# Kernel optimization log

Measured on AMD Instinct MI355X. Metric: run time of the kernel, lower is better.

## Reference

```python
import jax, jax.numpy as jnp
import numpy as np

MA_K = 25  # moving-average window for temporal pattern decoupling (trend extraction)
BN_EPS = 1e-5


def conv1d(x, w, b, dilation=1, padding=0, groups=1):
    # x: [N, C, L], w: [O, I/groups, K]
    out = jax.lax.conv_general_dilated(
        x, w, window_strides=(1,), padding=[(padding, padding)],
        rhs_dilation=(dilation,), dimension_numbers=("NCH", "OIH", "NCH"),
        feature_group_count=groups)
    if b is not None:
        out = out + b[None, :, None]
    return out


def moving_avg(x):
    # series-decomposition trend: depthwise uniform conv with edge padding
    c = x.shape[1]
    xp = jnp.pad(x, ((0, 0), (0, 0), (MA_K // 2, MA_K // 2)), mode="edge")
    k = jnp.full((c, 1, MA_K), 1.0 / MA_K, dtype=x.dtype)
    return conv1d(xp, k, None, dilation=1, padding=0, groups=c)


def setup_inputs() -> dict:
    key = jax.random.key(0)
    ks = jax.random.split(key, 12)
    B, C, L = 16, 256, 4096
    nb = 4
    c = C // nb  # 64 per branch
    inp = {
        "x": jax.random.normal(ks[0], (B, C, L), dtype=jnp.float32),
        # stacked per-branch Conv1dBlock params (all branches share c)
        "conv_w": jax.random.normal(ks[1], (nb, c, c, 3), dtype=jnp.float32) * 0.05,
        "conv_b": jax.random.normal(ks[2], (nb, c), dtype=jnp.float32) * 0.05,
        "bn_gamma": 1.0 + 0.1 * jax.random.normal(ks[3], (nb, c), dtype=jnp.float32),
        "bn_beta": 0.1 * jax.random.normal(ks[4], (nb, c), dtype=jnp.float32),
        "bn_mean": 0.1 * jax.random.normal(ks[5], (nb, c), dtype=jnp.float32),
        "bn_var": 0.5 + jax.random.uniform(ks[6], (nb, c), dtype=jnp.float32),
        # fusion 1x1 conv: 2C -> C
        "fusion_w": jax.random.normal(ks[7], (C, 2 * C, 1), dtype=jnp.float32) * 0.02,
        "fusion_b": jax.random.normal(ks[8], (C,), dtype=jnp.float32) * 0.02,
        "alpha": jnp.ones((1,), dtype=jnp.float32),
    }
    return inp


def reference(x, conv_w, conv_b, bn_gamma, bn_beta, bn_mean, bn_var,
              fusion_w, fusion_b, alpha):
    nb = conv_w.shape[0]
    parts = jnp.split(x, nb, axis=1)  # equal branch channels (C % nb == 0)
    shorts, longs = [], []
    for i in range(nb):
        d = 2 ** i  # dilation; padding = d keeps length for k=3
        h = conv1d(parts[i], conv_w[i], conv_b[i], dilation=d, padding=d)
        # BatchNorm1d, inference semantics (running stats)
        inv = jax.lax.rsqrt(bn_var[i] + BN_EPS)
        h = (h - bn_mean[i][None, :, None]) * (bn_gamma[i] * inv)[None, :, None] \
            + bn_beta[i][None, :, None]
        h = jax.nn.gelu(h, approximate=False)
        # TemporalPatternDecoupling: long = moving-average trend, short = residual
        l = moving_avg(h)
        s = h - l
        # dim_check AdaptiveAvgPool1d(seq_len) and F.interpolate(size=L) are
        # identity here since every branch already has length L == seq_len
        shorts.append(s)
        longs.append(l)
    # cumulative fuse: short forward, long backward
    for b in range(1, nb):
        shorts[b] = shorts[b] + shorts[b - 1]
    for b in reversed(range(nb - 1)):
        longs[b] = longs[b] + longs[b + 1]
    fused = jnp.concatenate(shorts + longs, axis=1)  # [B, 2C, L]
    out = jax.nn.relu(conv1d(fused, fusion_w, fusion_b))
    return out + alpha[0] * x
```

## Files before the change

kernel.cpp:

```cpp
#include <hip/hip_runtime.h>
#include <math.h>

#define BATCH 16
#define CCH 256
#define LSEQ 4096
#define NB 4
#define CB 64
#define MA_H 12
#define BN_EPS 1e-5f

typedef __attribute__((ext_vector_type(8))) short bf16x8;
typedef __attribute__((ext_vector_type(4))) float f32x4;

__device__ inline float b2f(ushort u) {
    union { uint i; float f; } v; v.i = ((uint)u) << 16; return v.f;
}
__device__ inline ushort f2b(float f) {
    uint x = __float_as_uint(f);
    return (ushort)((x + 0x7FFFu + ((x >> 16) & 1u)) >> 16);
}

__global__ __launch_bounds__(256) void k0w_fusionw(const float* __restrict__ fw,
                                                   ushort* __restrict__ wbf2)
{
    int e = blockIdx.x * 256 + threadIdx.x;
    int o = e >> 6, j = e & 63;
    const float* row = fw + (size_t)o * 512;
    float ws0 = row[j],       ws1 = row[64 + j],
          ws2 = row[128 + j], ws3 = row[192 + j];
    float wl0 = row[256 + j], wl1 = row[320 + j],
          wl2 = row[384 + j], wl3 = row[448 + j];
    float S3 = ws3, S2 = ws2 + S3, S1 = ws1 + S2, S0 = ws0 + S1;
    float L0 = wl0, L1 = L0 + wl1, L2 = L1 + wl2, L3 = L2 + wl3;
    ushort* dst = wbf2 + (size_t)o * 512;
    dst[j]        = f2b(S0); dst[64 + j]  = f2b(S1);
    dst[128 + j]  = f2b(S2); dst[192 + j] = f2b(S3);
    dst[256 + j]  = f2b(L0 - S0); dst[320 + j] = f2b(L1 - S1);
    dst[384 + j]  = f2b(L2 - S2); dst[448 + j] = f2b(L3 - S3);
}

__global__ __launch_bounds__(256) void k0b_convw_branch(
    const float* __restrict__ conv_w, ushort* __restrict__ wbr)
{
    int e = blockIdx.x * 256 + threadIdx.x;
    int i    = e & 63;
    int rest = e >> 6;
    int kk   = rest % 3;
    int orow = rest / 3;
    float v = conv_w[(size_t)orow * 192 + i * 3 + kk];
    wbr[(size_t)orow * 192 + kk * 64 + i] = f2b(v);
}

__global__ __launch_bounds__(256) void k0c_xT(const float* __restrict__ x,
                                              ushort* __restrict__ xT)
{
    const int p0    = blockIdx.x * 64;
    const int batch = blockIdx.y;
    const int tid   = threadIdx.x;

    __shared__ uint ls[256 * 33];

    const float* xb = x + (size_t)batch * CCH * LSEQ;
#pragma unroll
    for (int pass = 0; pass < 16; ++pass) {
        int e  = tid + pass * 256;
        int ch = e >> 4;
        int c4 = e & 15;
        float4 v = *(const float4*)&xb[(size_t)ch * LSEQ + p0 + c4 * 4];
        uint u0 = (uint)f2b(v.x) | ((uint)f2b(v.y) << 16);
        uint u1 = (uint)f2b(v.z) | ((uint)f2b(v.w) << 16);
        ls[ch * 33 + c4 * 2]     = u0;
        ls[ch * 33 + c4 * 2 + 1] = u1;
    }
    __syncthreads();

    const int w = tid >> 6, l = tid & 63;
    const ushort* lsu = (const ushort*)ls;
    ushort* dst = xT + ((size_t)batch * LSEQ + p0) * CCH;
#pragma unroll
    for (int r = 0; r < 16; ++r) {
        int p = w * 16 + r;
#pragma unroll
        for (int q = 0; q < 4; ++q) {
            int ch = l + 64 * q;
            dst[(size_t)p * CCH + ch] = lsu[ch * 66 + p];
        }
    }
}

#define SXA 72
#define SWB 200
__global__ __launch_bounds__(256) void k1_conv_mfma(
    const ushort* __restrict__ xT, const ushort* __restrict__ wbr,
    const float* __restrict__ conv_b, const float* __restrict__ bn_gamma,
    const float* __restrict__ bn_beta, const float* __restrict__ bn_mean,
    const float* __restrict__ bn_var, ushort* __restrict__ hT)
{
    const int tile  = blockIdx.x;
    const int br    = blockIdx.y;
    const int batch = blockIdx.z;
    const int d     = 1 << br;
    const int t0    = tile * 128;
    const int tid   = threadIdx.x;
    const int wm    = tid >> 6;
    const int lane  = tid & 63;
    const int lo    = lane & 15;
    const int hi    = lane >> 4;

    __shared__ ushort xsA[144 * SXA];
    __shared__ ushort wlB[64 * SWB];

    {
        const ushort* xTb = xT + (size_t)batch * LSEQ * CCH + br * CB;
#pragma unroll
        for (int pass = 0; pass < 5; ++pass) {
            int e = tid + pass * 256;
            int p = e >> 3;
            int c = e & 7;
            if (p < 144) {
                int gp = t0 - 8 + p;
                uint4 v = make_uint4(0u, 0u, 0u, 0u);
                if (gp >= 0 && gp < LSEQ)
                    v = *(const uint4*)&xTb[(size_t)gp * CCH + c * 8];
                *(uint4*)&xsA[p * SXA + c * 8] = v;
            }
        }
    }
    {
        const ushort* wrow = wbr + ((size_t)br * CB) * 192;
#pragma unroll
        for (int pass = 0; pass < 6; ++pass) {
            int e = tid + pass * 256;
            int o = e / 24;
            int c = e - o * 24;
            uint4 v = *(const uint4*)&wrow[e * 8];
            *(uint4*)&wlB[o * SWB + c * 8] = v;
        }
    }
    __syncthreads();

    f32x4 acc[2][4];
#pragma unroll
    for (int mi = 0; mi < 2; ++mi)
#pragma unroll
        for (int ni = 0; ni < 4; ++ni) acc[mi][ni] = (f32x4)0.f;

#pragma unroll
    for (int kk = 0; kk < 3; ++kk) {
        const int roff = 8 + (kk - 1) * d;
#pragma unroll
        for (int ks = 0; ks < 2; ++ks) {
            bf16x8 af[2], bfr[4];
#pragma unroll
            for (int mi = 0; mi < 2; ++mi)
                af[mi] = *(const bf16x8*)&xsA[
                    (wm * 32 + mi * 16 + lo + roff) * SXA + ks * 32 + hi * 8];
#pragma unroll
            for (int ni = 0; ni < 4; ++ni)
                bfr[ni] = *(const bf16x8*)&wlB[
                    (ni * 16 + lo) * SWB + kk * 64 + ks * 32 + hi * 8];
#pragma unroll
            for (int mi = 0; mi < 2; ++mi)
#pragma unroll
                for (int ni = 0; ni < 4; ++ni)
                    acc[mi][ni] = __builtin_amdgcn_mfma_f32_16x16x32_bf16(
                        af[mi], bfr[ni], acc[mi][ni], 0, 0, 0);
        }
    }

    __syncthreads();
    ushort* os = xsA;
#pragma unroll
    for (int ni = 0; ni < 4; ++ni) {
        const int o  = ni * 16 + lo;
        const int go = br * CB + o;
        float bias = conv_b[go];
        float inv  = rsqrtf(bn_var[go] + BN_EPS);
        float sc   = bn_gamma[go] * inv;
        float sh   = bn_beta[go] - bn_mean[go] * sc;
#pragma unroll
        for (int mi = 0; mi < 2; ++mi) {
            const int prow = wm * 32 + mi * 16 + hi * 4;
#pragma unroll
            for (int q = 0; q < 4; ++q) {
                float v = acc[mi][ni][q] + bias;
                v = v * sc + sh;
                os[(prow + q) * SXA + o] =
                    f2b(0.5f * v * (1.f + erff(v * 0.70710678118654752f)));
            }
        }
    }
    __syncthreads();
    ushort* hTb = hT + ((size_t)batch * LSEQ + t0) * CCH + br * CB;
#pragma unroll
    for (int pass = 0; pass < 4; ++pass) {
        int e = tid + pass * 256;
        int r = e >> 3;
        int c = e & 7;
        *(uint4*)&hTb[(size_t)r * CCH + c * 8] = *(const uint4*)&os[r * SXA + c * 8];
    }
}

#define LS_S 68
__global__ __launch_bounds__(256) void k2_ma(
    const ushort* __restrict__ hT, ushort* __restrict__ hmaT)
{
    const int p0    = blockIdx.x * 128;
    const int cg    = blockIdx.y;
    const int batch = blockIdx.z;
    const int tid   = threadIdx.x;

    __shared__ ushort ls[152 * LS_S];
    __shared__ ushort os[128 * LS_S];

    const ushort* src = hT + ((size_t)batch * LSEQ) * CCH + cg * 64;
#pragma unroll
    for (int pass = 0; pass < 10; ++pass) {
        int e = tid + pass * 256;
        int r = e >> 4;
        int c = e & 15;
        if (r < 152) {
            int gp = p0 - MA_H + r;
            gp = max(0, min(LSEQ - 1, gp));
            *(uint2*)&ls[r * LS_S + c * 4] = *(const uint2*)&src[(size_t)gp * CCH + c * 4];
        }
    }
    __syncthreads();

    const int ch = tid & 63;
    const int pg = tid >> 6;
    const int r0 = pg * 32;
    const float inv25 = 1.f / 25.f;

    float s = 0.f;
#pragma unroll
    for (int t = 0; t < 25; ++t) s += b2f(ls[(r0 + t) * LS_S + ch]);
    os[(r0 + 0) * LS_S + ch] = f2b(s * inv25);
#pragma unroll
    for (int t = 1; t < 32; ++t) {
        s += b2f(ls[(r0 + 24 + t) * LS_S + ch]) - b2f(ls[(r0 + t - 1) * LS_S + ch]);
        os[(r0 + t) * LS_S + ch] = f2b(s * inv25);
    }
    __syncthreads();

    ushort* dst = hmaT + ((size_t)batch * LSEQ + p0) * CCH + cg * 64;
#pragma unroll
    for (int pass = 0; pass < 8; ++pass) {
        int e = tid + pass * 256;
        int r = e >> 4;
        int c = e & 15;
        *(uint2*)&dst[(size_t)r * CCH + c * 4] = *(const uint2*)&os[r * LS_S + c * 4];
    }
}

#define KTOT 512
#define SA 72
__global__ __launch_bounds__(256) void k3_fusion(
    const ushort* __restrict__ hT, const ushort* __restrict__ hmaT,
    const ushort* __restrict__ wbf2, const float* __restrict__ fb,
    const float* __restrict__ x, const float* __restrict__ alpha,
    float* __restrict__ out)
{
    const int t0    = blockIdx.x * 128;
    const int oBase = blockIdx.y * 128;
    const int batch = blockIdx.z;
    const int tid   = threadIdx.x;
    const int wid   = tid >> 6;
    const int lane  = tid & 63;
    const int lo    = lane & 15;
    const int hi    = lane >> 4;
    const int wm    = wid >> 1;
    const int wn    = wid & 1;

    __shared__ short AL[128 * SA];
    __shared__ short WL[128 * SA];

    f32x4 acc[4][4];
#pragma unroll
    for (int mi = 0; mi < 4; ++mi)
#pragma unroll
        for (int ni = 0; ni < 4; ++ni) acc[mi][ni] = (f32x4)0.f;

    const int srow = tid >> 3;
    const int scol = tid & 7;

    for (int k0 = 0; k0 < KTOT; k0 += 64) {
        const ushort* asrc = (k0 < 256)
            ? hT   + ((size_t)(batch * LSEQ + t0)) * CCH + k0
            : hmaT + ((size_t)(batch * LSEQ + t0)) * CCH + (k0 - 256);
        __syncthreads();
#pragma unroll
        for (int pass = 0; pass < 4; ++pass) {
            int row = pass * 32 + srow;
            uint4 va = *(const uint4*)&asrc[(size_t)row * CCH + scol * 8];
            *(uint4*)&AL[row * SA + scol * 8] = va;
            uint4 vw = *(const uint4*)&wbf2[
                (size_t)(oBase + row) * KTOT + k0 + scol * 8];
            *(uint4*)&WL[row * SA + scol * 8] = vw;
        }
        __syncthreads();

#pragma unroll
        for (int ks = 0; ks < 2; ++ks) {
            bf16x8 af[4], bfr[4];
#pragma unroll
            for (int mi = 0; mi < 4; ++mi)
                af[mi] = *(const bf16x8*)&AL[(wm * 64 + mi * 16 + lo) * SA + ks * 32 + hi * 8];
#pragma unroll
            for (int ni = 0; ni < 4; ++ni)
                bfr[ni] = *(const bf16x8*)&WL[(wn * 64 + ni * 16 + lo) * SA + ks * 32 + hi * 8];
#pragma unroll
            for (int mi = 0; mi < 4; ++mi)
#pragma unroll
                for (int ni = 0; ni < 4; ++ni)
                    acc[mi][ni] = __builtin_amdgcn_mfma_f32_16x16x32_bf16(
                        af[mi], bfr[ni], acc[mi][ni], 0, 0, 0);
        }
    }

    const float al = alpha[0];
#pragma unroll
    for (int ni = 0; ni < 4; ++ni) {
        const int o = oBase + wn * 64 + ni * 16 + lo;
        const float bias = fb[o];
#pragma unroll
        for (int mi = 0; mi < 4; ++mi) {
            const int pos = t0 + wm * 64 + mi * 16 + hi * 4;
            size_t base = ((size_t)(batch * CCH + o)) * LSEQ + pos;
            float4 xv = *(const float4*)&x[base];
            float4 ov;
            ov.x = fmaxf(acc[mi][ni][0] + bias, 0.f) + al * xv.x;
            ov.y = fmaxf(acc[mi][ni][1] + bias, 0.f) + al * xv.y;
            ov.z = fmaxf(acc[mi][ni][2] + bias, 0.f) + al * xv.z;
            ov.w = fmaxf(acc[mi][ni][3] + bias, 0.f) + al * xv.w;
            *(float4*)&out[base] = ov;
        }
    }
}

extern "C" void kernel_launch(void* const* d_in, const int* in_sizes, int n_in,
                              void* d_out, int out_size, void* d_ws, size_t ws_size,
                              hipStream_t stream)
{
    const float* x        = (const float*)d_in[0];
    const float* conv_w   = (const float*)d_in[1];
    const float* conv_b   = (const float*)d_in[2];
    const float* bn_gamma = (const float*)d_in[3];
    const float* bn_beta  = (const float*)d_in[4];
    const float* bn_mean  = (const float*)d_in[5];
    const float* bn_var   = (const float*)d_in[6];
    const float* fw       = (const float*)d_in[7];
    const float* fb       = (const float*)d_in[8];
    const float* alpha    = (const float*)d_in[9];
    float* out = (float*)d_out;

    ushort* hT    = (ushort*)d_ws;
    ushort* hmaT  = (ushort*)((char*)d_ws + (size_t)32 * 1024 * 1024);
    ushort* wbf2  = (ushort*)((char*)d_ws + (size_t)96 * 1024 * 1024);
    ushort* wbr   = (ushort*)((char*)d_ws + (size_t)97 * 1024 * 1024);
    ushort* xT    = (ushort*)((char*)d_ws + (size_t)98 * 1024 * 1024);

    k0w_fusionw<<<dim3(64), 256, 0, stream>>>(fw, wbf2);
    k0b_convw_branch<<<dim3(192), 256, 0, stream>>>(conv_w, wbr);
    k0c_xT<<<dim3(64, 16), 256, 0, stream>>>(x, xT);

    dim3 g1(32, NB, BATCH);
    k1_conv_mfma<<<g1, 256, 0, stream>>>(xT, wbr, conv_b, bn_gamma, bn_beta,
                                         bn_mean, bn_var, hT);
    dim3 g2(32, 4, BATCH);
    k2_ma<<<g2, 256, 0, stream>>>(hT, hmaT);

    dim3 g3(32, 2, BATCH);
    k3_fusion<<<g3, 256, 0, stream>>>(hT, hmaT, wbf2, fb, x, alpha, out);
}
```

Baseline: 114.0 us.

## Make conv kernel persistent over four tiles with register-prefetched input

The dilated-conv MFMA kernel now handles four consecutive 128-position tiles per block instead of one, so the grid shrinks fourfold. Branch weights and the folded BN scale/shift are loaded once per block and reused across the tiles. The next tile's input rows are prefetched into registers while the current tile's MFMAs run. In exchange the grid has fewer blocks, which may hurt occupancy and latency hiding, and each tile now pays extra barriers and register pressure.

```diff
diff --git a/kernel.cpp b/kernel.cpp
--- a/kernel.cpp
+++ b/kernel.cpp
@@ -90,17 +90,16 @@
 
 #define SXA 72
 #define SWB 200
+#define K1T 4
 __global__ __launch_bounds__(256) void k1_conv_mfma(
     const ushort* __restrict__ xT, const ushort* __restrict__ wbr,
     const float* __restrict__ conv_b, const float* __restrict__ bn_gamma,
     const float* __restrict__ bn_beta, const float* __restrict__ bn_mean,
     const float* __restrict__ bn_var, ushort* __restrict__ hT)
 {
-    const int tile  = blockIdx.x;
     const int br    = blockIdx.y;
     const int batch = blockIdx.z;
     const int d     = 1 << br;
-    const int t0    = tile * 128;
     const int tid   = threadIdx.x;
     const int wm    = tid >> 6;
     const int lane  = tid & 63;
@@ -110,22 +109,8 @@
     __shared__ ushort xsA[144 * SXA];
     __shared__ ushort wlB[64 * SWB];
 
-    {
-        const ushort* xTb = xT + (size_t)batch * LSEQ * CCH + br * CB;
-#pragma unroll
-        for (int pass = 0; pass < 5; ++pass) {
-            int e = tid + pass * 256;
-            int p = e >> 3;
-            int c = e & 7;
-            if (p < 144) {
-                int gp = t0 - 8 + p;
-                uint4 v = make_uint4(0u, 0u, 0u, 0u);
-                if (gp >= 0 && gp < LSEQ)
-                    v = *(const uint4*)&xTb[(size_t)gp * CCH + c * 8];
-                *(uint4*)&xsA[p * SXA + c * 8] = v;
-            }
-        }
-    }
+    const ushort* xTb = xT + (size_t)batch * LSEQ * CCH + br * CB;
+
     {
         const ushort* wrow = wbr + ((size_t)br * CB) * 192;
 #pragma unroll
@@ -137,67 +122,112 @@
             *(uint4*)&wlB[o * SWB + c * 8] = v;
         }
     }
-    __syncthreads();
-
-    f32x4 acc[2][4];
-#pragma unroll
-    for (int mi = 0; mi < 2; ++mi)
-#pragma unroll
-        for (int ni = 0; ni < 4; ++ni) acc[mi][ni] = (f32x4)0.f;
-
-#pragma unroll
-    for (int kk = 0; kk < 3; ++kk) {
-        const int roff = 8 + (kk - 1) * d;
-#pragma unroll
-        for (int ks = 0; ks < 2; ++ks) {
-            bf16x8 af[2], bfr[4];
-#pragma unroll
-            for (int mi = 0; mi < 2; ++mi)
-                af[mi] = *(const bf16x8*)&xsA[
-                    (wm * 32 + mi * 16 + lo + roff) * SXA + ks * 32 + hi * 8];
-#pragma unroll
-            for (int ni = 0; ni < 4; ++ni)
-                bfr[ni] = *(const bf16x8*)&wlB[
-                    (ni * 16 + lo) * SWB + kk * 64 + ks * 32 + hi * 8];
-#pragma unroll
-            for (int mi = 0; mi < 2; ++mi)
+    float bias[4], sc[4], sh[4];
+#pragma unroll
+    for (int ni = 0; ni < 4; ++ni) {
+        const int go = br * CB + ni * 16 + lo;
+        bias[ni] = conv_b[go];
+        float inv = rsqrtf(bn_var[go] + BN_EPS);
+        sc[ni] = bn_gamma[go] * inv;
+        sh[ni] = bn_beta[go] - bn_mean[go] * sc[ni];
+    }
+
+    const int arow = tid >> 3;
+    const int acol = tid & 7;
+    uint4 areg[5];
+    {
+        const int t0 = blockIdx.x * (K1T * 128);
+#pragma unroll
+        for (int pass = 0; pass < 5; ++pass) {
+            int p = arow + pass * 32;
+            areg[pass] = make_uint4(0u, 0u, 0u, 0u);
+            if (p < 144) {
+                int gp = t0 - 8 + p;
+                if (gp >= 0 && gp < LSEQ)
+                    areg[pass] = *(const uint4*)&xTb[(size_t)gp * CCH + acol * 8];
+            }
+        }
+    }
+
+    for (int t = 0; t < K1T; ++t) {
+        const int t0 = blockIdx.x * (K1T * 128) + t * 128;
+        __syncthreads();
+#pragma unroll
+        for (int pass = 0; pass < 5; ++pass) {
+            int p = arow + pass * 32;
+            if (p < 144) *(uint4*)&xsA[p * SXA + acol * 8] = areg[pass];
+        }
+        __syncthreads();
+
+        f32x4 acc[2][4];
+#pragma unroll
+        for (int mi = 0; mi < 2; ++mi)
+#pragma unroll
+            for (int ni = 0; ni < 4; ++ni) acc[mi][ni] = (f32x4)0.f;
+
+#pragma unroll
+        for (int kk = 0; kk < 3; ++kk) {
+            const int roff = 8 + (kk - 1) * d;
+#pragma unroll
+            for (int ks = 0; ks < 2; ++ks) {
+                bf16x8 af[2], bfr[4];
+#pragma unroll
+                for (int mi = 0; mi < 2; ++mi)
+                    af[mi] = *(const bf16x8*)&xsA[
+                        (wm * 32 + mi * 16 + lo + roff) * SXA + ks * 32 + hi * 8];
 #pragma unroll
                 for (int ni = 0; ni < 4; ++ni)
-                    acc[mi][ni] = __builtin_amdgcn_mfma_f32_16x16x32_bf16(
-                        af[mi], bfr[ni], acc[mi][ni], 0, 0, 0);
-        }
-    }
-
-    __syncthreads();
-    ushort* os = xsA;
-#pragma unroll
-    for (int ni = 0; ni < 4; ++ni) {
-        const int o  = ni * 16 + lo;
-        const int go = br * CB + o;
-        float bias = conv_b[go];
-        float inv  = rsqrtf(bn_var[go] + BN_EPS);
-        float sc   = bn_gamma[go] * inv;
-        float sh   = bn_beta[go] - bn_mean[go] * sc;
-#pragma unroll
-        for (int mi = 0; mi < 2; ++mi) {
-            const int prow = wm * 32 + mi * 16 + hi * 4;
-#pragma unroll
-            for (int q = 0; q < 4; ++q) {
-                float v = acc[mi][ni][q] + bias;
-                v = v * sc + sh;
-                os[(prow + q) * SXA + o] =
-                    f2b(0.5f * v * (1.f + erff(v * 0.70710678118654752f)));
+                    bfr[ni] = *(const bf16x8*)&wlB[
+                        (ni * 16 + lo) * SWB + kk * 64 + ks * 32 + hi * 8];
+#pragma unroll
+                for (int mi = 0; mi < 2; ++mi)
+#pragma unroll
+                    for (int ni = 0; ni < 4; ++ni)
+                        acc[mi][ni] = __builtin_amdgcn_mfma_f32_16x16x32_bf16(
+                            af[mi], bfr[ni], acc[mi][ni], 0, 0, 0);
             }
         }
-    }
-    __syncthreads();
-    ushort* hTb = hT + ((size_t)batch * LSEQ + t0) * CCH + br * CB;
-#pragma unroll
-    for (int pass = 0; pass < 4; ++pass) {
-        int e = tid + pass * 256;
-        int r = e >> 3;
-        int c = e & 7;
-        *(uint4*)&hTb[(size_t)r * CCH + c * 8] = *(const uint4*)&os[r * SXA + c * 8];
+
+        if (t + 1 < K1T) {
+            const int tn = t0 + 128;
+#pragma unroll
+            for (int pass = 0; pass < 5; ++pass) {
+                int p = arow + pass * 32;
+                areg[pass] = make_uint4(0u, 0u, 0u, 0u);
+                if (p < 144) {
+                    int gp = tn - 8 + p;
+                    if (gp >= 0 && gp < LSEQ)
+                        areg[pass] = *(const uint4*)&xTb[(size_t)gp * CCH + acol * 8];
+                }
+            }
+        }
+
+        __syncthreads();
+        ushort* os = xsA;
+#pragma unroll
+        for (int ni = 0; ni < 4; ++ni) {
+            const int o = ni * 16 + lo;
+#pragma unroll
+            for (int mi = 0; mi < 2; ++mi) {
+                const int prow = wm * 32 + mi * 16 + hi * 4;
+#pragma unroll
+                for (int q = 0; q < 4; ++q) {
+                    float v = acc[mi][ni][q] + bias[ni];
+                    v = v * sc[ni] + sh[ni];
+                    os[(prow + q) * SXA + o] =
+                        f2b(0.5f * v * (1.f + erff(v * 0.70710678118654752f)));
+                }
+            }
+        }
+        __syncthreads();
+        ushort* hTb = hT + ((size_t)batch * LSEQ + t0) * CCH + br * CB;
+#pragma unroll
+        for (int pass = 0; pass < 4; ++pass) {
+            int e = tid + pass * 256;
+            int r = e >> 3;
+            int c = e & 7;
+            *(uint4*)&hTb[(size_t)r * CCH + c * 8] = *(const uint4*)&xsA[r * SXA + c * 8];
+        }
     }
 }
 
@@ -364,7 +394,7 @@
     k0b_convw_branch<<<dim3(192), 256, 0, stream>>>(conv_w, wbr);
     k0c_xT<<<dim3(64, 16), 256, 0, stream>>>(x, xT);
 
-    dim3 g1(32, NB, BATCH);
+    dim3 g1(8, NB, BATCH);
     k1_conv_mfma<<<g1, 256, 0, stream>>>(xT, wbr, conv_b, bn_gamma, bn_beta,
                                          bn_mean, bn_var, hT);
     dim3 g2(32, 4, BATCH);
```

New measurement: 109.7 us. 3.8% less time.
